# Optimization experiments

Measured on AMD Instinct MI355X. Metric: run time of the kernel, lower is better.

## Reference

```python
import jax, jax.numpy as jnp
import numpy as np

T, N, E = 32, 5000, 80000
F_IN, H, HD, NH, C = 128, 128, 512, 8, 10
DH = H // NH  # head dim
EPS = 1e-5


def _gcn_conv(x, src, dst, W, b):
    n = x.shape[0]
    loops = jnp.arange(n, dtype=src.dtype)
    s = jnp.concatenate([src, loops])
    d = jnp.concatenate([dst, loops])
    deg = jax.ops.segment_sum(jnp.ones_like(d, x.dtype), d, num_segments=n)
    dinv = jnp.where(deg > 0, jax.lax.rsqrt(deg), 0.0)
    h = x @ W  # [n, H]
    norm = dinv[s] * dinv[d]  # [e]
    out = jax.ops.segment_sum(h[s] * norm[:, None], d, num_segments=n)
    return out + b


def _graph_embed(x, ei, W0, b0, W1, b1, W2, b2):
    src, dst = ei[0], ei[1]
    h = jnp.tanh(_gcn_conv(x, src, dst, W0, b0))
    h = jnp.tanh(_gcn_conv(h, src, dst, W1, b1))
    h = jnp.tanh(_gcn_conv(h, src, dst, W2, b2))
    return jnp.sum(h, axis=0)  # SumAggregation over all nodes -> [H]


def _forward(x, edge_index, W0, b0, W1, b1, W2, b2,
             Wq, bq, Wk, bk, Wv, bv, Wo, bo,
             g2, beta2, Wm1, bm1, Wm2, bm2, Wl, bl):
    # per-graph GCN stack + sum aggregation -> [T, H]
    z = jax.vmap(_graph_embed, in_axes=(0, 0) + (None,) * 6)(
        x, edge_index, W0, b0, W1, b1, W2, b2)

    # unbatched multihead self-attention over the T sequence
    q = (z @ Wq + bq).reshape(T, NH, DH)
    k = (z @ Wk + bk).reshape(T, NH, DH)
    v = (z @ Wv + bv).reshape(T, NH, DH)
    scores = jnp.einsum('thd,shd->hts', q, k) / jnp.sqrt(jnp.asarray(DH, z.dtype))
    attn = jax.nn.softmax(scores, axis=-1)
    o = jnp.einsum('hts,shd->thd', attn, v).reshape(T, H)
    x_attend = o @ Wo + bo  # dropout1 is identity in eval
    # NOTE: layer_norm1 output is dead code in the original forward (assigned to x, never used)

    mlp = jax.nn.relu(x_attend @ Wm1 + bm1) @ Wm2 + bm2
    x_attend = x_attend + mlp  # dropout2 identity in eval

    mu = jnp.mean(x_attend, axis=-1, keepdims=True)
    var = jnp.var(x_attend, axis=-1, keepdims=True)
    x_attend = (x_attend - mu) * jax.lax.rsqrt(var + EPS) * g2 + beta2

    pooled = jnp.sum(jax.nn.relu(x_attend), axis=0)  # [H]
    return pooled @ Wl + bl  # [C]


def setup_inputs() -> dict:
    key = jax.random.key(0)
    ks = jax.random.split(key, 24)

    def lin(k, fan_in, shape):
        return jax.random.normal(k, shape, jnp.float32) / np.sqrt(fan_in)

    inp = {
        'x': jax.random.normal(ks[0], (T, N, F_IN), jnp.float32),
        'edge_index': jax.random.randint(ks[1], (T, 2, E), 0, N, jnp.int32),
        'W0': lin(ks[2], F_IN, (F_IN, H)), 'b0': jnp.zeros((H,), jnp.float32),
        'W1': lin(ks[3], H, (H, H)), 'b1': jnp.zeros((H,), jnp.float32),
        'W2': lin(ks[4], H, (H, H)), 'b2': jnp.zeros((H,), jnp.float32),
        'Wq': lin(ks[5], H, (H, H)), 'bq': jnp.zeros((H,), jnp.float32),
        'Wk': lin(ks[6], H, (H, H)), 'bk': jnp.zeros((H,), jnp.float32),
        'Wv': lin(ks[7], H, (H, H)), 'bv': jnp.zeros((H,), jnp.float32),
        'Wo': lin(ks[8], H, (H, H)), 'bo': jnp.zeros((H,), jnp.float32),
        'g2': jnp.ones((H,), jnp.float32), 'beta2': jnp.zeros((H,), jnp.float32),
        'Wm1': lin(ks[9], H, (H, HD)), 'bm1': jnp.zeros((HD,), jnp.float32),
        'Wm2': lin(ks[10], HD, (HD, H)), 'bm2': jnp.zeros((H,), jnp.float32),
        'Wl': lin(ks[11], H, (H, C)), 'bl': jnp.zeros((C,), jnp.float32),
    }
    return inp


def reference(x, edge_index, W0, b0, W1, b1, W2, b2,
              Wq, bq, Wk, bk, Wv, bv, Wo, bo,
              g2, beta2, Wm1, bm1, Wm2, bm2, Wl, bl):
    return _forward(x, edge_index, W0, b0, W1, b1, W2, b2,
                    Wq, bq, Wk, bk, Wv, bv, Wo, bo,
                    g2, beta2, Wm1, bm1, Wm2, bm2, Wl, bl)
```

## Files before the change

### kernel.cpp

```cpp
#include <hip/hip_runtime.h>
#include <cstdint>

#define T_ 32
#define N_ 5000
#define E_ 80000
#define H_ 128
#define HD_ 512
#define C_ 10

typedef _Float16 f16;
typedef f16 f16x8 __attribute__((ext_vector_type(8)));
typedef f16 f16x4 __attribute__((ext_vector_type(4)));
typedef f16 f16x2 __attribute__((ext_vector_type(2)));
typedef float f32x4 __attribute__((ext_vector_type(4)));

#define LDA 136
#define NB_ 8
#define EPS_ (E_ / NB_)
#define NBLK_ 313
#define GEMMB 768

__device__ inline int addpk(int a, int b) {
    f16x2 x = __builtin_bit_cast(f16x2, a);
    f16x2 y = __builtin_bit_cast(f16x2, b);
    f16x2 r = x + y;
    return __builtin_bit_cast(int, r);
}

__device__ inline float fast_tanh(float x) {
    return 1.0f - 2.0f / (__expf(2.0f * x) + 1.0f);
}

__device__ inline f16x8 cvt8(float4 a, float4 b) {
    return (f16x8){(f16)a.x, (f16)a.y, (f16)a.z, (f16)a.w,
                   (f16)b.x, (f16)b.y, (f16)b.z, (f16)b.w};
}

__global__ __launch_bounds__(256) void k_count(const int* __restrict__ ei, int* __restrict__ part) {
    __shared__ int cnt[N_];
    int blk = blockIdx.x;
    int t = blk & 31, seg = blk >> 5;
    int tid = threadIdx.x;
    for (int i = tid; i < N_; i += 256) cnt[i] = 0;
    __syncthreads();
    const int* dst = ei + (size_t)t * 2 * E_ + E_ + seg * EPS_;
    for (int e = tid * 4; e < EPS_; e += 1024) {
        int4 d = *(const int4*)&dst[e];
        atomicAdd(&cnt[d.x], 1);
        atomicAdd(&cnt[d.y], 1);
        atomicAdd(&cnt[d.z], 1);
        atomicAdd(&cnt[d.w], 1);
    }
    __syncthreads();
    int* p = part + (t * NB_ + seg) * N_;
    for (int i = tid * 4; i < N_; i += 1024) *(int4*)&p[i] = *(const int4*)&cnt[i];
}

__global__ __launch_bounds__(256) void k_scan(int* __restrict__ part, int* __restrict__ ptr,
                                              float* __restrict__ dinv, float* __restrict__ z) {
    __shared__ int cnt[N_];
    __shared__ int red[256];
    int t = blockIdx.x, tid = threadIdx.x;
    int base = t * N_;
    if (tid < 128) z[t * 128 + tid] = 0.0f;
    int* pp = part + t * NB_ * N_;

    for (int i = tid; i < N_; i += 256) {
        int c = 0;
#pragma unroll
        for (int s = 0; s < NB_; ++s) c += pp[s * N_ + i];
        cnt[i] = c;
        dinv[base + i] = rsqrtf((float)(c + 1));
    }
    __syncthreads();

    int vals[20];
    int sum = 0;
#pragma unroll
    for (int j = 0; j < 20; ++j) {
        int i = tid * 20 + j;
        int c = (i < N_) ? cnt[i] : 0;
        vals[j] = sum;
        sum += c;
    }
    red[tid] = sum;
    __syncthreads();
    for (int off = 1; off < 256; off <<= 1) {
        int v = (tid >= off) ? red[tid - off] : 0;
        __syncthreads();
        red[tid] += v;
        __syncthreads();
    }
    int prev = (tid > 0) ? red[tid - 1] : 0;
#pragma unroll
    for (int j = 0; j < 20; ++j) {
        int i = tid * 20 + j;
        if (i < N_) cnt[i] = prev + vals[j];
    }
    __syncthreads();

    for (int i = tid; i < N_; i += 256) {
        int run = cnt[i];
        ptr[base + i] = run;
#pragma unroll
        for (int s = 0; s < NB_; ++s) {
            int c = pp[s * N_ + i];
            pp[s * N_ + i] = run;
            run += c;
        }
    }
}

__global__ __launch_bounds__(256) void k_scatter(const int* __restrict__ ei,
                                                 const int* __restrict__ part,
                                                 uint16_t* __restrict__ col) {
    __shared__ int cur[N_];
    int blk = blockIdx.x;
    int t = blk & 31, seg = blk >> 5;
    int tid = threadIdx.x;
    const int* off = part + (t * NB_ + seg) * N_;
    for (int i = tid * 4; i < N_; i += 1024) *(int4*)&cur[i] = *(const int4*)&off[i];
    __syncthreads();
    const int* src = ei + (size_t)t * 2 * E_ + seg * EPS_;
    const int* dst = src + E_;
    uint16_t* cl = col + (size_t)t * E_;
    for (int e = tid * 4; e < EPS_; e += 1024) {
        int4 s4 = *(const int4*)&src[e];
        int4 d4 = *(const int4*)&dst[e];
        cl[atomicAdd(&cur[d4.x], 1)] = (uint16_t)s4.x;
        cl[atomicAdd(&cur[d4.y], 1)] = (uint16_t)s4.y;
        cl[atomicAdd(&cur[d4.z], 1)] = (uint16_t)s4.z;
        cl[atomicAdd(&cur[d4.w], 1)] = (uint16_t)s4.w;
    }
}

__global__ __launch_bounds__(256) void k_wprep(const float* __restrict__ W0,
                                               const float* __restrict__ W1,
                                               const float* __restrict__ W2,
                                               f16* __restrict__ Wt) {
    const float* W = (blockIdx.x == 0) ? W0 : (blockIdx.x == 1) ? W1 : W2;
    f16* dst = Wt + blockIdx.x * 16384;
    for (int idx = threadIdx.x; idx < 16384; idx += 256) {
        int c = idx >> 7, k = idx & 127;
        dst[idx] = (f16)W[k * 128 + c];
    }
}

template <bool F32IN>
__global__ __launch_bounds__(256, 3) void k_gemm(const void* __restrict__ in_,
                                                 const f16* __restrict__ Wt,
                                                 const float* __restrict__ dinv,
                                                 f16* __restrict__ g) {
    __shared__ f16 Ws[128 * LDA];
    __shared__ f16 slab[4][16 * LDA];
    int tid = threadIdx.x;
    {
        int c = tid >> 1, hf = tid & 1;
        const f16* src = Wt + c * 128 + hf * 64;
        f16* dst = Ws + c * LDA + hf * 64;
#pragma unroll
        for (int j = 0; j < 8; ++j) *(f16x8*)&dst[j * 8] = *(const f16x8*)&src[j * 8];
    }
    __syncthreads();

    int xc = blockIdx.x & 7;
    int jb = blockIdx.x >> 3;
    int w = tid >> 6, lane = tid & 63;
    int m = lane & 15, q = lane >> 4;
    int co = q * 8;
    f16* sl = slab[w];
    int srow = lane >> 4;
    int scol = (lane & 15) * 8;

    for (int task = jb * 4 + w; task < 4 * NBLK_; task += 384) {
        int gsel = task / NBLK_;
        int tile = task - gsel * NBLK_;
        int t = xc + (gsel << 3);
        int base = t * N_;
        int r0 = tile * 16;
        int rowA = r0 + m; if (rowA >= N_) rowA = N_ - 1;

        f16x8 a0, a1, a2, a3;
        if (F32IN) {
            const float* src = (const float*)in_ + (((size_t)(base + rowA)) << 7) + co;
            float4 u0 = *(const float4*)&src[0];
            float4 u1 = *(const float4*)&src[4];
            float4 u2 = *(const float4*)&src[32];
            float4 u3 = *(const float4*)&src[36];
            float4 u4 = *(const float4*)&src[64];
            float4 u5 = *(const float4*)&src[68];
            float4 u6 = *(const float4*)&src[96];
            float4 u7 = *(const float4*)&src[100];
            a0 = cvt8(u0, u1); a1 = cvt8(u2, u3); a2 = cvt8(u4, u5); a3 = cvt8(u6, u7);
        } else {
            const f16* src = (const f16*)in_ + (((size_t)(base + rowA)) << 7) + co;
            a0 = *(const f16x8*)&src[0];
            a1 = *(const f16x8*)&src[32];
            a2 = *(const f16x8*)&src[64];
            a3 = *(const f16x8*)&src[96];
        }

        f32x4 acc[8];
#pragma unroll
        for (int n = 0; n < 8; ++n) acc[n] = (f32x4){0.f, 0.f, 0.f, 0.f};
#pragma unroll
        for (int n = 0; n < 8; ++n) {
            f16x8 bF = *(const f16x8*)&Ws[(n * 16 + m) * LDA + co];
            acc[n] = __builtin_amdgcn_mfma_f32_16x16x32_f16(a0, bF, acc[n], 0, 0, 0);
        }
#pragma unroll
        for (int n = 0; n < 8; ++n) {
            f16x8 bF = *(const f16x8*)&Ws[(n * 16 + m) * LDA + 32 + co];
            acc[n] = __builtin_amdgcn_mfma_f32_16x16x32_f16(a1, bF, acc[n], 0, 0, 0);
        }
#pragma unroll
        for (int n = 0; n < 8; ++n) {
            f16x8 bF = *(const f16x8*)&Ws[(n * 16 + m) * LDA + 64 + co];
            acc[n] = __builtin_amdgcn_mfma_f32_16x16x32_f16(a2, bF, acc[n], 0, 0, 0);
        }
#pragma unroll
        for (int n = 0; n < 8; ++n) {
            f16x8 bF = *(const f16x8*)&Ws[(n * 16 + m) * LDA + 96 + co];
            acc[n] = __builtin_amdgcn_mfma_f32_16x16x32_f16(a3, bF, acc[n], 0, 0, 0);
        }

#pragma unroll
        for (int i = 0; i < 4; ++i) {
            int rr = q * 4 + i;
            int gr = r0 + rr; if (gr >= N_) gr = N_ - 1;
            float d = dinv[base + gr];
#pragma unroll
            for (int n = 0; n < 8; ++n)
                sl[rr * LDA + n * 16 + m] = (f16)(acc[n][i] * d);
        }
        asm volatile("s_waitcnt lgkmcnt(0)" ::: "memory");
#pragma unroll
        for (int j4 = 0; j4 < 4; ++j4) {
            int row = j4 * 4 + srow;
            f16x8 v = *(const f16x8*)&sl[row * LDA + scol];
            if (r0 + row < N_)
                *(f16x8*)&g[(((size_t)(base + r0 + row)) << 7) + scol] = v;
        }
    }
}

__global__ __launch_bounds__(256) void k_aggr(const int* __restrict__ ptr,
                                              const uint16_t* __restrict__ col,
                                              const f16* __restrict__ g,
                                              const float* __restrict__ dinv,
                                              const float* __restrict__ b,
                                              f16* __restrict__ out) {
    int x = blockIdx.x & 7;
    int j = blockIdx.x >> 3;
    int gsel = j / NBLK_;
    int nb = j - gsel * NBLK_;
    int t = x + (gsel << 3);

    int w = threadIdx.x >> 6;
    int lane = threadIdx.x & 63;
    int q = lane >> 4, m = lane & 15;
    int n0 = nb * 16 + w * 4;
    if (n0 >= N_) return;
    int base = t * N_;
    const f16* gg = g + (size_t)base * H_;
    const uint16_t* cl = col + (size_t)t * E_;
    int n = n0 + q;
    unsigned moB = (unsigned)(m * 8);

    int4 p4 = *(const int4*)&ptr[base + n0];
    int pend = (n0 + 4 < N_) ? ptr[base + n0 + 4] : E_;
    int begin = (q == 0) ? p4.x : (q == 1) ? p4.y : (q == 2) ? p4.z : p4.w;
    int end   = (q == 0) ? p4.y : (q == 1) ? p4.z : (q == 2) ? p4.w : pend;

    float dn = dinv[base + n];
    float4 b4a = *(const float4*)&b[m * 8];
    float4 b4b = *(const float4*)&b[m * 8 + 4];

    int zidx = 320000 - 5000 * t;

    f16x8 a0 = *(const f16x8*)&gg[((unsigned)n << 7) + moB];
    f16x8 a1 = {}, a2 = {}, a3 = {}, a4 = {}, a5 = {}, a6 = {}, a7 = {};

    int e0 = begin & ~7;
    int elast = (end - 1) & ~7;
    unsigned span = (unsigned)(end - begin);
    uint4 cc = *(const uint4*)&cl[e0];
    for (int e = e0; e < end; e += 8) {
        int en = e + 8;
        int epf = en < elast ? en : elast;
        uint4 cn = *(const uint4*)&cl[epf];
        unsigned eb = (unsigned)(e - begin);
        int i0 = (int)(cc.x & 0xFFFFu), i1 = (int)(cc.x >> 16);
        int i2 = (int)(cc.y & 0xFFFFu), i3 = (int)(cc.y >> 16);
        int i4 = (int)(cc.z & 0xFFFFu), i5 = (int)(cc.z >> 16);
        int i6 = (int)(cc.w & 0xFFFFu), i7 = (int)(cc.w >> 16);
        int s0 = (eb + 0 < span) ? i0 : zidx;
        int s1 = (eb + 1 < span) ? i1 : zidx;
        int s2 = (eb + 2 < span) ? i2 : zidx;
        int s3 = (eb + 3 < span) ? i3 : zidx;
        int s4 = (eb + 4 < span) ? i4 : zidx;
        int s5 = (eb + 5 < span) ? i5 : zidx;
        int s6 = (eb + 6 < span) ? i6 : zidx;
        int s7 = (eb + 7 < span) ? i7 : zidx;
        f16x8 v0 = *(const f16x8*)&gg[((unsigned)s0 << 7) + moB];
        f16x8 v1 = *(const f16x8*)&gg[((unsigned)s1 << 7) + moB];
        f16x8 v2 = *(const f16x8*)&gg[((unsigned)s2 << 7) + moB];
        f16x8 v3 = *(const f16x8*)&gg[((unsigned)s3 << 7) + moB];
        f16x8 v4 = *(const f16x8*)&gg[((unsigned)s4 << 7) + moB];
        f16x8 v5 = *(const f16x8*)&gg[((unsigned)s5 << 7) + moB];
        f16x8 v6 = *(const f16x8*)&gg[((unsigned)s6 << 7) + moB];
        f16x8 v7 = *(const f16x8*)&gg[((unsigned)s7 << 7) + moB];
        a0 += v0; a1 += v1; a2 += v2; a3 += v3;
        a4 += v4; a5 += v5; a6 += v6; a7 += v7;
        cc = cn;
    }
    a0 += a1; a2 += a3; a4 += a5; a6 += a7;
    a0 += a2; a4 += a6;
    a0 += a4;

    f16x8 o;
#pragma unroll
    for (int jj = 0; jj < 8; ++jj) {
        float bj = (jj < 4) ? ((const float*)&b4a)[jj] : ((const float*)&b4b)[jj - 4];
        o[jj] = (f16)fast_tanh(dn * (float)a0[jj] + bj);
    }
    *(f16x8*)&out[((size_t)base + n) * H_ + moB] = o;
}

__global__ __launch_bounds__(256) void k_reduce(const f16* __restrict__ h, float* __restrict__ z) {
    int t = blockIdx.x, seg = blockIdx.y;
    int tid = threadIdx.x;
    int rg = tid >> 5;
    int c = (tid & 31) * 4;
    const f16* p = h + (size_t)t * N_ * H_;
    float4 acc = make_float4(0.f, 0.f, 0.f, 0.f);
    int n0 = seg * 500;
    for (int n = n0 + rg; n < n0 + 500; n += 8) {
        f16x4 v = *(const f16x4*)&p[(size_t)n * H_ + c];
        acc.x += (float)v[0]; acc.y += (float)v[1]; acc.z += (float)v[2]; acc.w += (float)v[3];
    }
    __shared__ float4 part[256];
    part[tid] = acc;
    __syncthreads();
    if (rg == 0) {
        float4 s = part[tid];
#pragma unroll
        for (int j = 1; j < 8; ++j) {
            float4 v = part[(j << 5) + tid];
            s.x += v.x; s.y += v.y; s.z += v.z; s.w += v.w;
        }
        atomicAdd(&z[t * H_ + c + 0], s.x);
        atomicAdd(&z[t * H_ + c + 1], s.y);
        atomicAdd(&z[t * H_ + c + 2], s.z);
        atomicAdd(&z[t * H_ + c + 3], s.w);
    }
}

__global__ __launch_bounds__(128) void k_qkv(const float* __restrict__ z,
                                             const float* __restrict__ Wq, const float* __restrict__ bq,
                                             const float* __restrict__ Wk, const float* __restrict__ bk,
                                             const float* __restrict__ Wv, const float* __restrict__ bv,
                                             float* __restrict__ q, float* __restrict__ k,
                                             float* __restrict__ v) {
    int t = blockIdx.x, c = threadIdx.x;
    __shared__ float zs[128];
    zs[c] = z[t * 128 + c];
    __syncthreads();
    float aq = bq[c], ak = bk[c], av = bv[c];
    for (int kk = 0; kk < 128; ++kk) {
        float zv = zs[kk];
        aq += zv * Wq[(kk << 7) + c];
        ak += zv * Wk[(kk << 7) + c];
        av += zv * Wv[(kk << 7) + c];
    }
    q[t * 128 + c] = aq;
    k[t * 128 + c] = ak;
    v[t * 128 + c] = av;
}

__global__ __launch_bounds__(256) void k_attnmid(
    const float* __restrict__ q, const float* __restrict__ k, const float* __restrict__ v,
    const float* __restrict__ Wo, const float* __restrict__ bo,
    const float* __restrict__ g2, const float* __restrict__ beta2,
    const float* __restrict__ Wm1, const float* __restrict__ bm1,
    const float* __restrict__ Wm2, const float* __restrict__ bm2,
    float* __restrict__ xr) {
    int t = blockIdx.x, tid = threadIdx.x;
    __shared__ float Ks[32 * 128], Vs[32 * 128];
    __shared__ float qs[128], sc[8 * 32], xa[128], hid[512], ys[128];
    __shared__ float redA[128], redB[128];

    for (int i = tid; i < 32 * 128; i += 256) { Ks[i] = k[i]; Vs[i] = v[i]; }
    if (tid < 128) qs[tid] = q[t * 128 + tid];
    __syncthreads();

    {
        int h = tid >> 5, s = tid & 31;
        float d = 0.0f;
#pragma unroll
        for (int kk = 0; kk < 16; ++kk)
            d += qs[(h << 4) + kk] * Ks[(s << 7) + (h << 4) + kk];
        sc[tid] = d * 0.25f;
    }
    __syncthreads();
    if (tid < 8) {
        float m = -1e30f;
        for (int s = 0; s < 32; ++s) m = fmaxf(m, sc[(tid << 5) + s]);
        float l = 0.0f;
        for (int s = 0; s < 32; ++s) { float e = __expf(sc[(tid << 5) + s] - m); sc[(tid << 5) + s] = e; l += e; }
        float inv = 1.0f / l;
        for (int s = 0; s < 32; ++s) sc[(tid << 5) + s] *= inv;
    }
    __syncthreads();
    if (tid < 128) {
        int h = tid >> 4;
        float o = 0.0f;
        for (int s = 0; s < 32; ++s) o += sc[(h << 5) + s] * Vs[(s << 7) + tid];
        qs[tid] = o;
    }
    __syncthreads();
    if (tid < 128) {
        float a = bo[tid];
        for (int kk = 0; kk < 128; ++kk) a += qs[kk] * Wo[(kk << 7) + tid];
        xa[tid] = a;
    }
    __syncthreads();
    for (int j = tid; j < 512; j += 256) {
        float a = bm1[j];
        for (int kk = 0; kk < 128; ++kk) a += xa[kk] * Wm1[(kk << 9) + j];
        hid[j] = fmaxf(a, 0.0f);
    }
    __syncthreads();
    if (tid < 128) {
        float a = bm2[tid];
        for (int j = 0; j < 512; ++j) a += hid[j] * Wm2[(j << 7) + tid];
        ys[tid] = xa[tid] + a;
    }
    __syncthreads();
    if (tid < 128) { redA[tid] = ys[tid]; redB[tid] = ys[tid] * ys[tid]; }
    __syncthreads();
    for (int off = 64; off > 0; off >>= 1) {
        if (tid < off) { redA[tid] += redA[tid + off]; redB[tid] += redB[tid + off]; }
        __syncthreads();
    }
    float mu = redA[0] * (1.0f / 128.0f);
    float var = redB[0] * (1.0f / 128.0f) - mu * mu;
    float rs = rsqrtf(var + 1e-5f);
    if (tid < 128) {
        float yv = (ys[tid] - mu) * rs * g2[tid] + beta2[tid];
        xr[t * 128 + tid] = fmaxf(yv, 0.0f);
    }
}

__global__ __launch_bounds__(128) void k_final(const float* __restrict__ xr,
                                               const float* __restrict__ Wl,
                                               const float* __restrict__ bl,
                                               float* __restrict__ out) {
    int tid = threadIdx.x;
    __shared__ float pooled[128];
    float s = 0.0f;
    for (int t = 0; t < 32; ++t) s += xr[t * 128 + tid];
    pooled[tid] = s;
    __syncthreads();
    if (tid < C_) {
        float a = bl[tid];
        for (int kk = 0; kk < 128; ++kk) a += pooled[kk] * Wl[kk * C_ + tid];
        out[tid] = a;
    }
}

extern "C" void kernel_launch(void* const* d_in, const int* in_sizes, int n_in,
                              void* d_out, int out_size, void* d_ws, size_t ws_size,
                              hipStream_t stream) {
    const float* x  = (const float*)d_in[0];
    const int*   ei = (const int*)d_in[1];
    const float* W0 = (const float*)d_in[2];  const float* b0 = (const float*)d_in[3];
    const float* W1 = (const float*)d_in[4];  const float* b1 = (const float*)d_in[5];
    const float* W2 = (const float*)d_in[6];  const float* b2 = (const float*)d_in[7];
    const float* Wq = (const float*)d_in[8];  const float* bq = (const float*)d_in[9];
    const float* Wk = (const float*)d_in[10]; const float* bk = (const float*)d_in[11];
    const float* Wv = (const float*)d_in[12]; const float* bv = (const float*)d_in[13];
    const float* Wo = (const float*)d_in[14]; const float* bo = (const float*)d_in[15];
    const float* g2 = (const float*)d_in[16]; const float* beta2 = (const float*)d_in[17];
    const float* Wm1 = (const float*)d_in[18]; const float* bm1 = (const float*)d_in[19];
    const float* Wm2 = (const float*)d_in[20]; const float* bm2 = (const float*)d_in[21];
    const float* Wl = (const float*)d_in[22]; const float* bl = (const float*)d_in[23];
    float* outp = (float*)d_out;

    const size_t BIG = (size_t)T_ * N_ * H_;
    char* ws = (char*)d_ws;
    float*    dinv = (float*)(ws);
    int*      ptr  = (int*)(ws + 640000);
    uint16_t* col  = (uint16_t*)(ws + 1280000);
    f16*      Wt   = (f16*)(ws + 6400000);
    f16*      P16  = (f16*)(ws + 6498304);
    f16*      Q16  = P16 + BIG;
    float*    z    = (float*)(Q16 + BIG);
    float*    zq   = z + 4096;
    float*    zk   = zq + 4096;
    float*    zv   = zk + 4096;
    float*    xr   = zv + 4096;
    int*      part = (int*)P16;

    k_wprep<<<3, 256, 0, stream>>>(W0, W1, W2, Wt);
    k_count<<<NB_ * 32, 256, 0, stream>>>(ei, part);
    k_scan<<<T_, 256, 0, stream>>>(part, ptr, dinv, z);
    k_scatter<<<NB_ * 32, 256, 0, stream>>>(ei, part, col);

    const float* bl_[3] = {b0, b1, b2};
    const int AGGR_BLOCKS = NBLK_ * 32;
    k_gemm<true><<<GEMMB, 256, 0, stream>>>(x, Wt, dinv, P16);
    k_aggr<<<AGGR_BLOCKS, 256, 0, stream>>>(ptr, col, P16, dinv, bl_[0], Q16);
    k_gemm<false><<<GEMMB, 256, 0, stream>>>(Q16, Wt + 16384, dinv, P16);
    k_aggr<<<AGGR_BLOCKS, 256, 0, stream>>>(ptr, col, P16, dinv, bl_[1], Q16);
    k_gemm<false><<<GEMMB, 256, 0, stream>>>(Q16, Wt + 32768, dinv, P16);
    k_aggr<<<AGGR_BLOCKS, 256, 0, stream>>>(ptr, col, P16, dinv, bl_[2], Q16);

    k_reduce<<<dim3(T_, 10), 256, 0, stream>>>(Q16, z);

    k_qkv<<<T_, 128, 0, stream>>>(z, Wq, bq, Wk, bk, Wv, bv, zq, zk, zv);
    k_attnmid<<<T_, 256, 0, stream>>>(zq, zk, zv, Wo, bo, g2, beta2,
                                      Wm1, bm1, Wm2, bm2, xr);
    k_final<<<1, 128, 0, stream>>>(xr, Wl, bl, outp);
}
```

Before: 488.5 us.

## Fuse GCN aggregation with next layer's weight GEMM per 16-row tile

Layers one and two now run the neighbour aggregation plus tanh, stage the 16-row tile in shared memory, and immediately multiply by the next layer's weights with MFMA, scaled by dinv. The output goes to the ping-pong buffer, which removes two standalone GEMM launches and the round trip of the hidden activations through global memory. The zero-row index is passed per layer because the buffers alternate. In exchange, each block adds two barriers and reads the 32KB weight matrix from global memory per tile, and it requests a launch bound of 3 blocks per CU.

```diff
diff --git a/kernel.cpp b/kernel.cpp
--- a/kernel.cpp
+++ b/kernel.cpp
@@ -15,17 +15,11 @@
 typedef float f32x4 __attribute__((ext_vector_type(4)));
 
 #define LDA 136
+#define LDH 136
 #define NB_ 8
 #define EPS_ (E_ / NB_)
 #define NBLK_ 313
 #define GEMMB 768
-
-__device__ inline int addpk(int a, int b) {
-    f16x2 x = __builtin_bit_cast(f16x2, a);
-    f16x2 y = __builtin_bit_cast(f16x2, b);
-    f16x2 r = x + y;
-    return __builtin_bit_cast(int, r);
-}
 
 __device__ inline float fast_tanh(float x) {
     return 1.0f - 2.0f / (__expf(2.0f * x) + 1.0f);
@@ -244,26 +238,32 @@
     }
 }
 
-__global__ __launch_bounds__(256) void k_aggr(const int* __restrict__ ptr,
-                                              const uint16_t* __restrict__ col,
-                                              const f16* __restrict__ g,
-                                              const float* __restrict__ dinv,
-                                              const float* __restrict__ b,
-                                              f16* __restrict__ out) {
+__global__ __launch_bounds__(256, 3) void k_fused(const int* __restrict__ ptr,
+                                                  const uint16_t* __restrict__ col,
+                                                  const f16* __restrict__ g,
+                                                  const float* __restrict__ dinv,
+                                                  const float* __restrict__ b,
+                                                  const f16* __restrict__ Wn,
+                                                  int zbase,
+                                                  f16* __restrict__ out) {
+    __shared__ f16 hs[16 * LDH];
+    __shared__ f16 ot[16 * LDH];
     int x = blockIdx.x & 7;
     int j = blockIdx.x >> 3;
     int gsel = j / NBLK_;
     int nb = j - gsel * NBLK_;
     int t = x + (gsel << 3);
 
-    int w = threadIdx.x >> 6;
-    int lane = threadIdx.x & 63;
+    int tid = threadIdx.x;
+    int w = tid >> 6;
+    int lane = tid & 63;
     int q = lane >> 4, m = lane & 15;
-    int n0 = nb * 16 + w * 4;
-    if (n0 >= N_) return;
     int base = t * N_;
     const f16* gg = g + (size_t)base * H_;
     const uint16_t* cl = col + (size_t)t * E_;
+    int r0 = nb * 16;
+    int n0 = r0 + w * 4;
+    if (n0 > N_ - 4) n0 = N_ - 4;
     int n = n0 + q;
     unsigned moB = (unsigned)(m * 8);
 
@@ -276,7 +276,7 @@
     float4 b4a = *(const float4*)&b[m * 8];
     float4 b4b = *(const float4*)&b[m * 8 + 4];
 
-    int zidx = 320000 - 5000 * t;
+    int zidx = zbase - 5000 * t;
 
     f16x8 a0 = *(const f16x8*)&gg[((unsigned)n << 7) + moB];
     f16x8 a1 = {}, a2 = {}, a3 = {}, a4 = {}, a5 = {}, a6 = {}, a7 = {};
@@ -324,6 +324,117 @@
         float bj = (jj < 4) ? ((const float*)&b4a)[jj] : ((const float*)&b4b)[jj - 4];
         o[jj] = (f16)fast_tanh(dn * (float)a0[jj] + bj);
     }
+    *(f16x8*)&hs[(w * 4 + q) * LDH + m * 8] = o;
+    __syncthreads();
+
+    f32x4 acc0 = (f32x4){0.f, 0.f, 0.f, 0.f};
+    f32x4 acc1 = (f32x4){0.f, 0.f, 0.f, 0.f};
+#pragma unroll
+    for (int kb = 0; kb < 4; ++kb) {
+        f16x8 aF = *(const f16x8*)&hs[m * LDH + kb * 32 + q * 8];
+        f16x8 b0F = *(const f16x8*)&Wn[(w * 32 + m) * 128 + kb * 32 + q * 8];
+        f16x8 b1F = *(const f16x8*)&Wn[(w * 32 + 16 + m) * 128 + kb * 32 + q * 8];
+        acc0 = __builtin_amdgcn_mfma_f32_16x16x32_f16(aF, b0F, acc0, 0, 0, 0);
+        acc1 = __builtin_amdgcn_mfma_f32_16x16x32_f16(aF, b1F, acc1, 0, 0, 0);
+    }
+#pragma unroll
+    for (int i = 0; i < 4; ++i) {
+        int rr = q * 4 + i;
+        int gr = r0 + rr; if (gr >= N_) gr = N_ - 1;
+        float d = dinv[base + gr];
+        ot[rr * LDH + w * 32 + m]      = (f16)(acc0[i] * d);
+        ot[rr * LDH + w * 32 + 16 + m] = (f16)(acc1[i] * d);
+    }
+    __syncthreads();
+    {
+        int row = tid >> 4, c8 = (tid & 15) * 8;
+        if (r0 + row < N_) {
+            f16x8 v = *(const f16x8*)&ot[row * LDH + c8];
+            *(f16x8*)&out[((size_t)(base + r0 + row)) * H_ + c8] = v;
+        }
+    }
+}
+
+__global__ __launch_bounds__(256) void k_aggr(const int* __restrict__ ptr,
+                                              const uint16_t* __restrict__ col,
+                                              const f16* __restrict__ g,
+                                              const float* __restrict__ dinv,
+                                              const float* __restrict__ b,
+                                              f16* __restrict__ out) {
+    int x = blockIdx.x & 7;
+    int j = blockIdx.x >> 3;
+    int gsel = j / NBLK_;
+    int nb = j - gsel * NBLK_;
+    int t = x + (gsel << 3);
+
+    int w = threadIdx.x >> 6;
+    int lane = threadIdx.x & 63;
+    int q = lane >> 4, m = lane & 15;
+    int n0 = nb * 16 + w * 4;
+    if (n0 >= N_) return;
+    int base = t * N_;
+    const f16* gg = g + (size_t)base * H_;
+    const uint16_t* cl = col + (size_t)t * E_;
+    int n = n0 + q;
+    unsigned moB = (unsigned)(m * 8);
+
+    int4 p4 = *(const int4*)&ptr[base + n0];
+    int pend = (n0 + 4 < N_) ? ptr[base + n0 + 4] : E_;
+    int begin = (q == 0) ? p4.x : (q == 1) ? p4.y : (q == 2) ? p4.z : p4.w;
+    int end   = (q == 0) ? p4.y : (q == 1) ? p4.z : (q == 2) ? p4.w : pend;
+
+    float dn = dinv[base + n];
+    float4 b4a = *(const float4*)&b[m * 8];
+    float4 b4b = *(const float4*)&b[m * 8 + 4];
+
+    int zidx = 320000 - 5000 * t;
+
+    f16x8 a0 = *(const f16x8*)&gg[((unsigned)n << 7) + moB];
+    f16x8 a1 = {}, a2 = {}, a3 = {}, a4 = {}, a5 = {}, a6 = {}, a7 = {};
+
+    int e0 = begin & ~7;
+    int elast = (end - 1) & ~7;
+    unsigned span = (unsigned)(end - begin);
+    uint4 cc = *(const uint4*)&cl[e0];
+    for (int e = e0; e < end; e += 8) {
+        int en = e + 8;
+        int epf = en < elast ? en : elast;
+        uint4 cn = *(const uint4*)&cl[epf];
+        unsigned eb = (unsigned)(e - begin);
+        int i0 = (int)(cc.x & 0xFFFFu), i1 = (int)(cc.x >> 16);
+        int i2 = (int)(cc.y & 0xFFFFu), i3 = (int)(cc.y >> 16);
+        int i4 = (int)(cc.z & 0xFFFFu), i5 = (int)(cc.z >> 16);
+        int i6 = (int)(cc.w & 0xFFFFu), i7 = (int)(cc.w >> 16);
+        int s0 = (eb + 0 < span) ? i0 : zidx;
+        int s1 = (eb + 1 < span) ? i1 : zidx;
+        int s2 = (eb + 2 < span) ? i2 : zidx;
+        int s3 = (eb + 3 < span) ? i3 : zidx;
+        int s4 = (eb + 4 < span) ? i4 : zidx;
+        int s5 = (eb + 5 < span) ? i5 : zidx;
+        int s6 = (eb + 6 < span) ? i6 : zidx;
+        int s7 = (eb + 7 < span) ? i7 : zidx;
+        f16x8 v0 = *(const f16x8*)&gg[((unsigned)s0 << 7) + moB];
+        f16x8 v1 = *(const f16x8*)&gg[((unsigned)s1 << 7) + moB];
+        f16x8 v2 = *(const f16x8*)&gg[((unsigned)s2 << 7) + moB];
+        f16x8 v3 = *(const f16x8*)&gg[((unsigned)s3 << 7) + moB];
+        f16x8 v4 = *(const f16x8*)&gg[((unsigned)s4 << 7) + moB];
+        f16x8 v5 = *(const f16x8*)&gg[((unsigned)s5 << 7) + moB];
+        f16x8 v6 = *(const f16x8*)&gg[((unsigned)s6 << 7) + moB];
+        f16x8 v7 = *(const f16x8*)&gg[((unsigned)s7 << 7) + moB];
+        a0 += v0; a1 += v1; a2 += v2; a3 += v3;
+        a4 += v4; a5 += v5; a6 += v6; a7 += v7;
+        cc = cn;
+    }
+    a0 += a1; a2 += a3; a4 += a5; a6 += a7;
+    a0 += a2; a4 += a6;
+    a0 += a4;
+
+    f16x8 o;
+#pragma unroll
+    for (int jj = 0; jj < 8; ++jj) {
+        float bj = (jj < 4) ? ((const float*)&b4a)[jj] : ((const float*)&b4b)[jj - 4];
+        o[jj] = (f16)fast_tanh(dn * (float)a0[jj] + bj);
+    }
     *(f16x8*)&out[((size_t)base + n) * H_ + moB] = o;
 }
 
@@ -507,14 +618,11 @@
     k_scan<<<T_, 256, 0, stream>>>(part, ptr, dinv, z);
     k_scatter<<<NB_ * 32, 256, 0, stream>>>(ei, part, col);
 
-    const float* bl_[3] = {b0, b1, b2};
     const int AGGR_BLOCKS = NBLK_ * 32;
     k_gemm<true><<<GEMMB, 256, 0, stream>>>(x, Wt, dinv, P16);
-    k_aggr<<<AGGR_BLOCKS, 256, 0, stream>>>(ptr, col, P16, dinv, bl_[0], Q16);
-    k_gemm<false><<<GEMMB, 256, 0, stream>>>(Q16, Wt + 16384, dinv, P16);
-    k_aggr<<<AGGR_BLOCKS, 256, 0, stream>>>(ptr, col, P16, dinv, bl_[1], Q16);
-    k_gemm<false><<<GEMMB, 256, 0, stream>>>(Q16, Wt + 32768, dinv, P16);
-    k_aggr<<<AGGR_BLOCKS, 256, 0, stream>>>(ptr, col, P16, dinv, bl_[2], Q16);
+    k_fused<<<AGGR_BLOCKS, 256, 0, stream>>>(ptr, col, P16, dinv, b0, Wt + 16384, 320000, Q16);
+    k_fused<<<AGGR_BLOCKS, 256, 0, stream>>>(ptr, col, Q16, dinv, b1, Wt + 32768, 160000, P16);
+    k_aggr<<<AGGR_BLOCKS, 256, 0, stream>>>(ptr, col, P16, dinv, b2, Q16);
 
     k_reduce<<<dim3(T_, 10), 256, 0, stream>>>(Q16, z);
 
```

After: 526.4 us. 7.8% more time.
